# Performance work log

Hardware: AMD Instinct MI355X
Metric: run time of the kernel (lower is better)

The kernel has to match this reference:

```python
import jax, jax.numpy as jnp
import numpy as np

N = 50000      # n_samples (nodes)
F = 128        # n_features
H = 32         # hidden_dim
C = 16         # code_dim
DEG = 32       # avg degree
E = N * DEG + N  # random edges + self loops


def setup_inputs() -> dict:
    key = jax.random.key(0)
    ks = jax.random.split(key, 9)
    src = jax.random.randint(ks[0], (N * DEG,), 0, N, dtype=jnp.int32)
    dst = jax.random.randint(ks[1], (N * DEG,), 0, N, dtype=jnp.int32)
    loops = jnp.arange(N, dtype=jnp.int32)
    edge_src = jnp.concatenate([src, loops])
    edge_dst = jnp.concatenate([dst, loops])
    # symmetric normalization D^{-1/2} (A+I) D^{-1/2} on the edge list
    deg = jax.ops.segment_sum(jnp.ones((E,), jnp.float32), edge_dst, num_segments=N)
    deg = jnp.maximum(deg, 1.0)
    edge_w = jax.lax.rsqrt(deg[edge_src] * deg[edge_dst])
    rand_u = jax.random.uniform(ks[2], (N, C), jnp.float32)  # torch.rand_like
    def w(k, i, o):
        return jax.random.normal(k, (i, o), jnp.float32) * (1.0 / np.sqrt(i))
    return {
        'x': jax.random.normal(ks[3], (N, F), jnp.float32),
        'edge_src': edge_src, 'edge_dst': edge_dst, 'edge_w': edge_w,
        'rand_u': rand_u,
        'W1': w(ks[4], F, H), 'Wm': w(ks[5], H, C), 'Ws': w(ks[6], H, C),
        'Wd': w(ks[7], C, H), 'Wo': w(ks[8], H, F),
    }


def _gcn(x, W, edge_src, edge_dst, edge_w):
    # KipfAndWillingConv: spmm(A_norm, x @ W)
    support = x @ W                               # [N, out]
    msgs = edge_w[:, None] * support[edge_src]    # [E, out]
    return jax.ops.segment_sum(msgs, edge_dst, num_segments=N)


def reference(x, edge_src, edge_dst, edge_w, rand_u, W1, Wm, Ws, Wd, Wo):
    gcn = lambda h, W: _gcn(h, W, edge_src, edge_dst, edge_w)
    hidden = jax.nn.relu(gcn(x, W1))
    means = gcn(hidden, Wm)
    std = jax.nn.elu(gcn(hidden, Ws)) + 1.0
    encoded = means + std * rand_u                # uniform reparameterization
    decoded = jax.nn.relu(gcn(encoded, Wd))
    prediction = jax.nn.relu(gcn(decoded, Wo))
    return (prediction, means, std)
```

## Files before the change

### kernel.cpp

```cpp
#include <hip/hip_runtime.h>
#include <hip/hip_bf16.h>
#include <hip/hip_fp16.h>

typedef unsigned int u32;
typedef unsigned short u16;
typedef unsigned long long u64;

#define NBIN 512
#define BSH 7
#define BCAP 36
#define CHUNK 4096
#define PAD 80
#define HB 128

__global__ __launch_bounds__(64) void k_init(int* __restrict__ ovf_cnt) {
  if (threadIdx.x == 0) *ovf_cnt = 0;
}

__global__ __launch_bounds__(512) void k_bin(const int* __restrict__ src, const int* __restrict__ dst,
                                             int E2, u32* __restrict__ binned, int* __restrict__ blkcnt,
                                             u32* __restrict__ ovf, int* __restrict__ ovf_cnt, int ovfcap) {
  __shared__ int curs[NBIN];
  const int p = blockIdx.x;
  const int base = p * CHUNK;
  const int len = min(CHUNK, E2 - base);
  const int t = threadIdx.x;
  const int lane = t & 63;
  for (int i = t; i < NBIN; i += 512) curs[i] = 0;
  __syncthreads();
  const u32 blkBase = (u32)p * (NBIN * BCAP);
  for (int i = t; i < len; i += 512) {
    int d = dst[base + i];
    u32 e = ((u32)d << 16) | (u32)src[base + i];
    int b = d >> BSH;
    int pos = atomicAdd(&curs[b], 1);
    if (pos < BCAP) binned[blkBase + (u32)b * BCAP + pos] = e;
    u64 om = __ballot(pos >= BCAP);
    if (om) {
      int leader = __ffsll((long long)om) - 1;
      int ob = 0;
      if (lane == leader) ob = atomicAdd(ovf_cnt, (int)__popcll(om));
      ob = __shfl(ob, leader);
      if (pos >= BCAP) {
        int oi = ob + (int)__popcll(om & ((1ull << lane) - 1ull));
        if (oi < ovfcap) ovf[oi] = e;
      }
    }
  }
  __syncthreads();
  for (int b = t; b < NBIN; b += 512) blkcnt[p * NBIN + b] = min(curs[b], BCAP);
}

__global__ __launch_bounds__(512) void k_sort(const u32* __restrict__ binned, const int* __restrict__ blkcnt,
                                              int nblk, const u32* __restrict__ ovf,
                                              const int* __restrict__ ovf_cnt, int N,
                                              u16* __restrict__ csr, int* __restrict__ cur) {
  __shared__ __attribute__((aligned(16))) u16 scsr[HB * PAD];
  __shared__ int cnt[HB];
  const int bin = blockIdx.x;
  const int lo = bin << BSH;
  if (lo >= N) return;
  const int hi = min(lo + HB, N);
  const int H = hi - lo;
  const int t = threadIdx.x;
  const int w = t >> 6, lane = t & 63;
  for (int i = t; i < HB; i += 512) cnt[i] = 0;
  __syncthreads();
  const int per = (nblk + 7) / 8;
  const int c0 = w * per;
  const int c1 = min(nblk, c0 + per);
  const int s = lane >> 3;
  const int k = lane & 7;
  for (int p = c0; p < c1; p += 8) {
    const int myp = p + s;
    int len = 0; u32 sb = 0;
    if (myp < c1) {
      len = blkcnt[myp * NBIN + bin];
      sb = ((u32)myp * NBIN + (u32)bin) * BCAP;
    }
    for (int i = k; i < len; i += 8) {
      u32 e = binned[sb + i];
      int d = (int)(e >> 16);
      int pos = atomicAdd(&cnt[d - lo], 1);
      if (pos < PAD) scsr[(d - lo) * PAD + pos] = (u16)(e & 0xffffu);
    }
  }
  const int onum = min(*ovf_cnt, 1 << 19);
  for (int i = t; i < onum; i += 512) {
    u32 e = ovf[i];
    int d = (int)(e >> 16);
    if (d >= lo && d < hi) {
      int pos = atomicAdd(&cnt[d - lo], 1);
      if (pos < PAD) scsr[(d - lo) * PAD + pos] = (u16)(e & 0xffffu);
    }
  }
  __syncthreads();
  if (H == HB) {
    const uint4* s4 = (const uint4*)scsr;
    uint4* d4 = (uint4*)(csr + (size_t)lo * PAD);
    for (int i = t; i < HB * PAD / 8; i += 512) d4[i] = s4[i];
  } else {
    for (int i = t; i < H * (PAD / 8); i += 512) {
      int node = i / (PAD / 8), q = i % (PAD / 8);
      ((uint4*)(csr + (size_t)(lo + node) * PAD))[q] = ((const uint4*)(scsr + node * PAD))[q];
    }
  }
  for (int i = t; i < H; i += 512) cur[lo + i] = cnt[i];
}

__device__ __forceinline__ void acc8(uint4 v, float* a) {
  const __half2* h = reinterpret_cast<const __half2*>(&v);
#pragma unroll
  for (int p = 0; p < 4; ++p) {
    float2 f = __half22float2(h[p]);
    a[2 * p] += f.x;
    a[2 * p + 1] += f.y;
  }
}
__device__ __forceinline__ uint4 pack8h(const float* v) {
  uint4 r;
  __half2* h = reinterpret_cast<__half2*>(&r);
#pragma unroll
  for (int p = 0; p < 4; ++p) h[p] = __floats2half2_rn(v[2 * p], v[2 * p + 1]);
  return r;
}
__device__ __forceinline__ uint2 pack4h(const float* v) {
  uint2 r;
  __half2* h = reinterpret_cast<__half2*>(&r);
  h[0] = __floats2half2_rn(v[0], v[1]);
  h[1] = __floats2half2_rn(v[2], v[3]);
  return r;
}

template <int LPN8>
__device__ __forceinline__ void gather8h(const u16* __restrict__ csr, const int* __restrict__ cur,
                                         const float* __restrict__ dinv, const uint4* __restrict__ supv,
                                         int g, int cg, float* acc, float& dg_out) {
  int len = min(cur[g], PAD);
  const u16* c = csr + (size_t)g * PAD;
#pragma unroll
  for (int p = 0; p < 8; ++p) acc[p] = 0.f;
  acc8(supv[(size_t)g * LPN8 + cg], acc);
  int i = 0;
  for (; i + 3 < len; i += 4) {
    ushort4 ii = *(const ushort4*)(c + i);
    acc8(supv[(size_t)ii.x * LPN8 + cg], acc);
    acc8(supv[(size_t)ii.y * LPN8 + cg], acc);
    acc8(supv[(size_t)ii.z * LPN8 + cg], acc);
    acc8(supv[(size_t)ii.w * LPN8 + cg], acc);
  }
  for (; i < len; ++i) acc8(supv[(size_t)c[i] * LPN8 + cg], acc);
  float dg = dinv[g];
  dg_out = dg;
#pragma unroll
  for (int p = 0; p < 8; ++p) acc[p] *= dg;
}

__global__ __launch_bounds__(256) void k_spmm_relu(const u16* __restrict__ csr, const int* __restrict__ cur,
                                                   const float* __restrict__ dinv,
                                                   const uint4* __restrict__ sup, uint4* __restrict__ out, int N) {
  int g = blockIdx.x * 64 + (int)(threadIdx.x >> 2);
  int cg = threadIdx.x & 3;
  if (g >= N) return;
  float a[8], dg;
  gather8h<4>(csr, cur, dinv, sup, g, cg, a, dg);
#pragma unroll
  for (int p = 0; p < 8; ++p) a[p] = dg * fmaxf(a[p], 0.f);
  out[(size_t)g * 4 + cg] = pack8h(a);
}

__global__ __launch_bounds__(256) void k_spmm_ms(const u16* __restrict__ csr, const int* __restrict__ cur,
                                                  const float* __restrict__ dinv,
                                                  const uint4* __restrict__ sup,
                                                  const float* __restrict__ Wm, const float* __restrict__ Ws,
                                                  const float* __restrict__ ru,
                                                  uint2* __restrict__ enc,
                                                  float* __restrict__ o_means, float* __restrict__ o_std, int N) {
  __shared__ float w[32 * 32];
  __shared__ float aggT[64][33];
  const int t = threadIdx.x;
  for (int i = t; i < 32 * 32; i += 256) {
    int k = i >> 5, j = i & 31;
    w[i] = (j < 16) ? Wm[k * 16 + j] : Ws[k * 16 + (j - 16)];
  }
  const int n = t >> 2;
  const int q = t & 3;
  const int g = blockIdx.x * 64 + n;
  const bool act = g < N;
  float dg = 0.f, a[8];
  if (act) {
    gather8h<4>(csr, cur, dinv, sup, g, q, a, dg);
#pragma unroll
    for (int p = 0; p < 8; ++p) aggT[n][q * 8 + p] = a[p];
  }
  __syncthreads();
  if (act) {
    float4 rm = make_float4(0.f, 0.f, 0.f, 0.f);
    float4 rs = make_float4(0.f, 0.f, 0.f, 0.f);
    for (int k = 0; k < 32; ++k) {
      float rv = aggT[n][k];
      const float4* wr = (const float4*)&w[k * 32];
      float4 wm = wr[q];
      float4 wsv = wr[4 + q];
      rm.x += rv * wm.x; rm.y += rv * wm.y; rm.z += rv * wm.z; rm.w += rv * wm.w;
      rs.x += rv * wsv.x; rs.y += rv * wsv.y; rs.z += rv * wsv.z; rs.w += rv * wsv.w;
    }
    ((float4*)o_means)[(size_t)g * 4 + q] = rm;
    rs.x = ((rs.x > 0.f) ? rs.x : expm1f(rs.x)) + 1.0f;
    rs.y = ((rs.y > 0.f) ? rs.y : expm1f(rs.y)) + 1.0f;
    rs.z = ((rs.z > 0.f) ? rs.z : expm1f(rs.z)) + 1.0f;
    rs.w = ((rs.w > 0.f) ? rs.w : expm1f(rs.w)) + 1.0f;
    ((float4*)o_std)[(size_t)g * 4 + q] = rs;
    float4 uu = ((const float4*)ru)[(size_t)g * 4 + q];
    float e[4] = {dg * (rm.x + rs.x * uu.x), dg * (rm.y + rs.y * uu.y),
                  dg * (rm.z + rs.z * uu.z), dg * (rm.w + rs.w * uu.w)};
    enc[(size_t)g * 4 + q] = pack4h(e);
  }
}

__global__ __launch_bounds__(256) void k_spmm_d(const u16* __restrict__ csr, const int* __restrict__ cur,
                                                 const float* __restrict__ dinv,
                                                 const uint4* __restrict__ sup,
                                                 const float* __restrict__ Wd,
                                                 uint2* __restrict__ out, int N) {
  __shared__ float w[16 * 32];
  __shared__ float aggT[128][17];
  const int t = threadIdx.x;
  for (int i = t; i < 16 * 32; i += 256) w[i] = Wd[i];
  const int n = t >> 1;
  const int q = t & 1;
  const int g = blockIdx.x * 128 + n;
  const bool act = g < N;
  float dg = 0.f, a[8];
  if (act) {
    gather8h<2>(csr, cur, dinv, sup, g, q, a, dg);
#pragma unroll
    for (int p = 0; p < 8; ++p) aggT[n][q * 8 + p] = a[p];
  }
  __syncthreads();
  if (act) {
    float4 r4[4];
#pragma unroll
    for (int h = 0; h < 4; ++h) r4[h] = make_float4(0.f, 0.f, 0.f, 0.f);
    for (int k = 0; k < 16; ++k) {
      float rv = aggT[n][k];
      const float4* wr = (const float4*)&w[k * 32];
#pragma unroll
      for (int h = 0; h < 4; ++h) {
        float4 wv = wr[q + 2 * h];
        r4[h].x += rv * wv.x; r4[h].y += rv * wv.y;
        r4[h].z += rv * wv.z; r4[h].w += rv * wv.w;
      }
    }
#pragma unroll
    for (int h = 0; h < 4; ++h) {
      float v[4] = {dg * fmaxf(r4[h].x, 0.f), dg * fmaxf(r4[h].y, 0.f),
                    dg * fmaxf(r4[h].z, 0.f), dg * fmaxf(r4[h].w, 0.f)};
      out[(size_t)g * 8 + q + 2 * h] = pack4h(v);
    }
  }
}

__global__ __launch_bounds__(256) void k_spmm_o(const u16* __restrict__ csr, const int* __restrict__ cur,
                                                 const float* __restrict__ dinv,
                                                 const uint4* __restrict__ sup,
                                                 const float* __restrict__ Wo,
                                                 float* __restrict__ out, int N) {
  __shared__ float w[32 * 128];
  __shared__ float aggT[64][33];
  const int t = threadIdx.x;
  for (int i = t; i < 32 * 128; i += 256) w[i] = Wo[i];
  const int n = t >> 2;
  const int q = t & 3;
  const int g = blockIdx.x * 64 + n;
  const bool act = g < N;
  float dg, a[8];
  if (act) {
    gather8h<4>(csr, cur, dinv, sup, g, q, a, dg);
#pragma unroll
    for (int p = 0; p < 8; ++p) aggT[n][q * 8 + p] = a[p];
  }
  __syncthreads();
  if (act) {
    float4 r4[8];
#pragma unroll
    for (int h = 0; h < 8; ++h) r4[h] = make_float4(0.f, 0.f, 0.f, 0.f);
    for (int k = 0; k < 32; ++k) {
      float rv = aggT[n][k];
      const float4* wr = (const float4*)&w[k * 128];
#pragma unroll
      for (int h = 0; h < 8; ++h) {
        float4 wv = wr[q + 4 * h];
        r4[h].x += rv * wv.x; r4[h].y += rv * wv.y;
        r4[h].z += rv * wv.z; r4[h].w += rv * wv.w;
      }
    }
    float4* orow = (float4*)(out + (size_t)g * 128);
#pragma unroll
    for (int h = 0; h < 8; ++h)
      orow[q + 4 * h] = make_float4(fmaxf(r4[h].x, 0.f), fmaxf(r4[h].y, 0.f),
                                    fmaxf(r4[h].z, 0.f), fmaxf(r4[h].w, 0.f));
  }
}

__global__ __launch_bounds__(256) void k_mm1(const float* __restrict__ x, const float* __restrict__ W1,
                                             const int* __restrict__ cur, float* __restrict__ dinv,
                                             uint4* __restrict__ out, int N) {
  __shared__ float w[128 * 32];
  for (int i = threadIdx.x; i < 128 * 32; i += 256) w[i] = W1[i];
  __syncthreads();
  int n = blockIdx.x * 256 + threadIdx.x;
  if (n >= N) return;
  float dn = rsqrtf((float)(cur[n] + 1));
  dinv[n] = dn;
  const float4* xr = (const float4*)(x + (size_t)n * 128);
  float acc[32];
#pragma unroll
  for (int j = 0; j < 32; ++j) acc[j] = 0.f;
  for (int kb = 0; kb < 32; ++kb) {
    float4 p = xr[kb];
    float xe[4] = {p.x, p.y, p.z, p.w};
#pragma unroll
    for (int h = 0; h < 4; ++h) {
      float xv = xe[h];
      const float4* wr = (const float4*)&w[(kb * 4 + h) * 32];
#pragma unroll
      for (int q = 0; q < 8; ++q) {
        float4 a = wr[q];
        acc[q * 4 + 0] += xv * a.x; acc[q * 4 + 1] += xv * a.y;
        acc[q * 4 + 2] += xv * a.z; acc[q * 4 + 3] += xv * a.w;
      }
    }
  }
#pragma unroll
  for (int j = 0; j < 32; ++j) acc[j] *= dn;
  uint4* o = out + (size_t)n * 4;
#pragma unroll
  for (int q = 0; q < 4; ++q) o[q] = pack8h(&acc[q * 8]);
}

extern "C" void kernel_launch(void* const* d_in, const int* in_sizes, int n_in,
                              void* d_out, int out_size, void* d_ws, size_t ws_size,
                              hipStream_t stream) {
  const float* x  = (const float*)d_in[0];
  const int* esrc = (const int*)d_in[1];
  const int* edst = (const int*)d_in[2];
  const float* ru = (const float*)d_in[4];
  const float* W1 = (const float*)d_in[5];
  const float* Wm = (const float*)d_in[6];
  const float* Ws = (const float*)d_in[7];
  const float* Wd = (const float*)d_in[8];
  const float* Wo = (const float*)d_in[9];
  const int N = in_sizes[0] / 128;
  const int E = in_sizes[1];
  const int E2 = E - N;

  const int nblk = (E2 + CHUNK - 1) / CHUNK;
  const int ovfcap = 1 << 19;

  char* ws = (char*)d_ws;
  size_t off = 0;
  auto alloc = [&](size_t bytes) {
    void* p = ws + off;
    off = (off + bytes + 255) & ~(size_t)255;
    return p;
  };
  u16*   csr     = (u16*)alloc((size_t)N * PAD * 2);
  u32*   binned  = (u32*)alloc((size_t)nblk * NBIN * BCAP * 4);
  int*   blkcnt  = (int*)alloc((size_t)nblk * NBIN * 4);
  u32*   ovf     = (u32*)alloc((size_t)ovfcap * 4);
  int*   ovf_cnt = (int*)alloc(256);
  int*   cur     = (int*)alloc((size_t)N * 4);
  float* dinv    = (float*)alloc((size_t)N * 4);
  uint4* h0      = (uint4*)alloc((size_t)N * 32 * 2);
  uint4* h1      = (uint4*)alloc((size_t)N * 32 * 2);
  uint2* henc    = (uint2*)alloc((size_t)N * 16 * 2);

  float* out_pred  = (float*)d_out;
  float* out_means = out_pred + (size_t)N * 128;
  float* out_std   = out_means + (size_t)N * 16;

  const int nb = (N + 255) / 256;
  const int sortBlocks = (N + HB - 1) / HB;
  const int g64 = (N + 63) / 64;
  const int g128 = (N + 127) / 128;

  k_init<<<1, 64, 0, stream>>>(ovf_cnt);
  k_bin<<<nblk, 512, 0, stream>>>(esrc, edst, E2, binned, blkcnt, ovf, ovf_cnt, ovfcap);
  k_sort<<<sortBlocks, 512, 0, stream>>>(binned, blkcnt, nblk, ovf, ovf_cnt, N, csr, cur);

  k_mm1<<<nb, 256, 0, stream>>>(x, W1, cur, dinv, h0, N);
  k_spmm_relu<<<g64, 256, 0, stream>>>(csr, cur, dinv, h0, h1, N);
  k_spmm_ms<<<g64, 256, 0, stream>>>(csr, cur, dinv, h1, Wm, Ws, ru,
                                     henc, out_means, out_std, N);
  k_spmm_d<<<g128, 256, 0, stream>>>(csr, cur, dinv, (const uint4*)henc, Wd,
                                     (uint2*)h0, N);
  k_spmm_o<<<g64, 256, 0, stream>>>(csr, cur, dinv, h0, Wo, out_pred, N);
}
```

Measured before the change: 149.1 us.

## Split each node's neighbor gather across two thread halves with shuffle reduction

```diff
diff --git a/kernel.cpp b/kernel.cpp
--- a/kernel.cpp
+++ b/kernel.cpp
@@ -131,26 +131,34 @@
   h[1] = __floats2half2_rn(v[2], v[3]);
   return r;
 }
-
-template <int LPN8>
-__device__ __forceinline__ void gather8h(const u16* __restrict__ csr, const int* __restrict__ cur,
-                                         const float* __restrict__ dinv, const uint4* __restrict__ supv,
-                                         int g, int cg, float* acc, float& dg_out) {
+__device__ __forceinline__ u32 pack2h(float a, float b) {
+  __half2 h = __floats2half2_rn(a, b);
+  return *reinterpret_cast<u32*>(&h);
+}
+
+template <int LPN, int XD>
+__device__ __forceinline__ void gather_split(const u16* __restrict__ csr, const int* __restrict__ cur,
+                                             const float* __restrict__ dinv, const uint4* __restrict__ supv,
+                                             int g, int cg, int half, float* acc, float& dg_out) {
   int len = min(cur[g], PAD);
   const u16* c = csr + (size_t)g * PAD;
 #pragma unroll
   for (int p = 0; p < 8; ++p) acc[p] = 0.f;
-  acc8(supv[(size_t)g * LPN8 + cg], acc);
-  int i = 0;
-  for (; i + 3 < len; i += 4) {
-    ushort4 ii = *(const ushort4*)(c + i);
-    acc8(supv[(size_t)ii.x * LPN8 + cg], acc);
-    acc8(supv[(size_t)ii.y * LPN8 + cg], acc);
-    acc8(supv[(size_t)ii.z * LPN8 + cg], acc);
-    acc8(supv[(size_t)ii.w * LPN8 + cg], acc);
-  }
-  for (; i < len; ++i) acc8(supv[(size_t)c[i] * LPN8 + cg], acc);
+  if (half == 0) acc8(supv[(size_t)g * LPN + cg], acc);
+  const int full4 = len >> 2;
+  for (int j = half; j < full4; j += 2) {
+    ushort4 ii = *(const ushort4*)(c + 4 * j);
+    acc8(supv[(size_t)ii.x * LPN + cg], acc);
+    acc8(supv[(size_t)ii.y * LPN + cg], acc);
+    acc8(supv[(size_t)ii.z * LPN + cg], acc);
+    acc8(supv[(size_t)ii.w * LPN + cg], acc);
+  }
+  if ((full4 & 1) == half) {
+    for (int i = full4 << 2; i < len; ++i) acc8(supv[(size_t)c[i] * LPN + cg], acc);
+  }
   float dg = dinv[g];
+#pragma unroll
+  for (int p = 0; p < 8; ++p) acc[p] += __shfl_xor(acc[p], XD);
   dg_out = dg;
 #pragma unroll
   for (int p = 0; p < 8; ++p) acc[p] *= dg;
@@ -159,14 +167,17 @@
 __global__ __launch_bounds__(256) void k_spmm_relu(const u16* __restrict__ csr, const int* __restrict__ cur,
                                                    const float* __restrict__ dinv,
                                                    const uint4* __restrict__ sup, uint4* __restrict__ out, int N) {
-  int g = blockIdx.x * 64 + (int)(threadIdx.x >> 2);
-  int cg = threadIdx.x & 3;
+  int g = blockIdx.x * 32 + (int)(threadIdx.x >> 3);
+  int sub = threadIdx.x & 7;
+  int half = sub >> 2, cg = sub & 3;
   if (g >= N) return;
   float a[8], dg;
-  gather8h<4>(csr, cur, dinv, sup, g, cg, a, dg);
-#pragma unroll
-  for (int p = 0; p < 8; ++p) a[p] = dg * fmaxf(a[p], 0.f);
-  out[(size_t)g * 4 + cg] = pack8h(a);
+  gather_split<4, 4>(csr, cur, dinv, sup, g, cg, half, a, dg);
+  if (half == 0) {
+#pragma unroll
+    for (int p = 0; p < 8; ++p) a[p] = dg * fmaxf(a[p], 0.f);
+    out[(size_t)g * 4 + cg] = pack8h(a);
+  }
 }
 
 __global__ __launch_bounds__(256) void k_spmm_ms(const u16* __restrict__ csr, const int* __restrict__ cur,
@@ -174,47 +185,45 @@
                                                   const uint4* __restrict__ sup,
                                                   const float* __restrict__ Wm, const float* __restrict__ Ws,
                                                   const float* __restrict__ ru,
-                                                  uint2* __restrict__ enc,
+                                                  u32* __restrict__ enc,
                                                   float* __restrict__ o_means, float* __restrict__ o_std, int N) {
   __shared__ float w[32 * 32];
-  __shared__ float aggT[64][33];
+  __shared__ float aggT[32][33];
   const int t = threadIdx.x;
   for (int i = t; i < 32 * 32; i += 256) {
     int k = i >> 5, j = i & 31;
     w[i] = (j < 16) ? Wm[k * 16 + j] : Ws[k * 16 + (j - 16)];
   }
-  const int n = t >> 2;
-  const int q = t & 3;
-  const int g = blockIdx.x * 64 + n;
+  const int n = t >> 3;
+  const int sub = t & 7;
+  const int half = sub >> 2, cg = sub & 3;
+  const int g = blockIdx.x * 32 + n;
   const bool act = g < N;
   float dg = 0.f, a[8];
   if (act) {
-    gather8h<4>(csr, cur, dinv, sup, g, q, a, dg);
-#pragma unroll
-    for (int p = 0; p < 8; ++p) aggT[n][q * 8 + p] = a[p];
-  }
-  __syncthreads();
-  if (act) {
-    float4 rm = make_float4(0.f, 0.f, 0.f, 0.f);
-    float4 rs = make_float4(0.f, 0.f, 0.f, 0.f);
+    gather_split<4, 4>(csr, cur, dinv, sup, g, cg, half, a, dg);
+    if (half == 0) {
+#pragma unroll
+      for (int p = 0; p < 8; ++p) aggT[n][cg * 8 + p] = a[p];
+    }
+  }
+  __syncthreads();
+  if (act) {
+    const int q = sub;
+    float2 rm = make_float2(0.f, 0.f), rs = make_float2(0.f, 0.f);
     for (int k = 0; k < 32; ++k) {
       float rv = aggT[n][k];
-      const float4* wr = (const float4*)&w[k * 32];
-      float4 wm = wr[q];
-      float4 wsv = wr[4 + q];
-      rm.x += rv * wm.x; rm.y += rv * wm.y; rm.z += rv * wm.z; rm.w += rv * wm.w;
-      rs.x += rv * wsv.x; rs.y += rv * wsv.y; rs.z += rv * wsv.z; rs.w += rv * wsv.w;
-    }
-    ((float4*)o_means)[(size_t)g * 4 + q] = rm;
+      const float2* wr = (const float2*)&w[k * 32];
+      float2 wm = wr[q], wsv = wr[8 + q];
+      rm.x += rv * wm.x; rm.y += rv * wm.y;
+      rs.x += rv * wsv.x; rs.y += rv * wsv.y;
+    }
+    ((float2*)o_means)[(size_t)g * 8 + q] = rm;
     rs.x = ((rs.x > 0.f) ? rs.x : expm1f(rs.x)) + 1.0f;
     rs.y = ((rs.y > 0.f) ? rs.y : expm1f(rs.y)) + 1.0f;
-    rs.z = ((rs.z > 0.f) ? rs.z : expm1f(rs.z)) + 1.0f;
-    rs.w = ((rs.w > 0.f) ? rs.w : expm1f(rs.w)) + 1.0f;
-    ((float4*)o_std)[(size_t)g * 4 + q] = rs;
-    float4 uu = ((const float4*)ru)[(size_t)g * 4 + q];
-    float e[4] = {dg * (rm.x + rs.x * uu.x), dg * (rm.y + rs.y * uu.y),
-                  dg * (rm.z + rs.z * uu.z), dg * (rm.w + rs.w * uu.w)};
-    enc[(size_t)g * 4 + q] = pack4h(e);
+    ((float2*)o_std)[(size_t)g * 8 + q] = rs;
+    float2 uu = ((const float2*)ru)[(size_t)g * 8 + q];
+    enc[(size_t)g * 8 + q] = pack2h(dg * (rm.x + rs.x * uu.x), dg * (rm.y + rs.y * uu.y));
   }
 }
 
@@ -224,40 +233,40 @@
                                                  const float* __restrict__ Wd,
                                                  uint2* __restrict__ out, int N) {
   __shared__ float w[16 * 32];
-  __shared__ float aggT[128][17];
+  __shared__ float aggT[64][17];
   const int t = threadIdx.x;
   for (int i = t; i < 16 * 32; i += 256) w[i] = Wd[i];
-  const int n = t >> 1;
-  const int q = t & 1;
-  const int g = blockIdx.x * 128 + n;
+  const int n = t >> 2;
+  const int sub = t & 3;
+  const int half = sub >> 1, cg = sub & 1;
+  const int g = blockIdx.x * 64 + n;
   const bool act = g < N;
   float dg = 0.f, a[8];
   if (act) {
-    gather8h<2>(csr, cur, dinv, sup, g, q, a, dg);
-#pragma unroll
-    for (int p = 0; p < 8; ++p) aggT[n][q * 8 + p] = a[p];
-  }
-  __syncthreads();
-  if (act) {
-    float4 r4[4];
-#pragma unroll
-    for (int h = 0; h < 4; ++h) r4[h] = make_float4(0.f, 0.f, 0.f, 0.f);
+    gather_split<2, 2>(csr, cur, dinv, sup, g, cg, half, a, dg);
+    if (half == 0) {
+#pragma unroll
+      for (int p = 0; p < 8; ++p) aggT[n][cg * 8 + p] = a[p];
+    }
+  }
+  __syncthreads();
+  if (act) {
+    const int q = sub;
+    float4 r0 = make_float4(0.f, 0.f, 0.f, 0.f), r1 = r0;
     for (int k = 0; k < 16; ++k) {
       float rv = aggT[n][k];
       const float4* wr = (const float4*)&w[k * 32];
-#pragma unroll
-      for (int h = 0; h < 4; ++h) {
-        float4 wv = wr[q + 2 * h];
-        r4[h].x += rv * wv.x; r4[h].y += rv * wv.y;
-        r4[h].z += rv * wv.z; r4[h].w += rv * wv.w;
-      }
-    }
-#pragma unroll
-    for (int h = 0; h < 4; ++h) {
-      float v[4] = {dg * fmaxf(r4[h].x, 0.f), dg * fmaxf(r4[h].y, 0.f),
-                    dg * fmaxf(r4[h].z, 0.f), dg * fmaxf(r4[h].w, 0.f)};
-      out[(size_t)g * 8 + q + 2 * h] = pack4h(v);
-    }
+      float4 w0 = wr[q], w1 = wr[q + 4];
+      r0.x += rv * w0.x; r0.y += rv * w0.y; r0.z += rv * w0.z; r0.w += rv * w0.w;
+      r1.x += rv * w1.x; r1.y += rv * w1.y; r1.z += rv * w1.z; r1.w += rv * w1.w;
+    }
+    float v[4];
+    v[0] = dg * fmaxf(r0.x, 0.f); v[1] = dg * fmaxf(r0.y, 0.f);
+    v[2] = dg * fmaxf(r0.z, 0.f); v[3] = dg * fmaxf(r0.w, 0.f);
+    out[(size_t)g * 8 + q] = pack4h(v);
+    v[0] = dg * fmaxf(r1.x, 0.f); v[1] = dg * fmaxf(r1.y, 0.f);
+    v[2] = dg * fmaxf(r1.z, 0.f); v[3] = dg * fmaxf(r1.w, 0.f);
+    out[(size_t)g * 8 + q + 4] = pack4h(v);
   }
 }
 
@@ -267,38 +276,42 @@
                                                  const float* __restrict__ Wo,
                                                  float* __restrict__ out, int N) {
   __shared__ float w[32 * 128];
-  __shared__ float aggT[64][33];
+  __shared__ float aggT[32][33];
   const int t = threadIdx.x;
   for (int i = t; i < 32 * 128; i += 256) w[i] = Wo[i];
-  const int n = t >> 2;
-  const int q = t & 3;
-  const int g = blockIdx.x * 64 + n;
+  const int n = t >> 3;
+  const int sub = t & 7;
+  const int half = sub >> 2, cg = sub & 3;
+  const int g = blockIdx.x * 32 + n;
   const bool act = g < N;
   float dg, a[8];
   if (act) {
-    gather8h<4>(csr, cur, dinv, sup, g, q, a, dg);
-#pragma unroll
-    for (int p = 0; p < 8; ++p) aggT[n][q * 8 + p] = a[p];
-  }
-  __syncthreads();
-  if (act) {
-    float4 r4[8];
-#pragma unroll
-    for (int h = 0; h < 8; ++h) r4[h] = make_float4(0.f, 0.f, 0.f, 0.f);
+    gather_split<4, 4>(csr, cur, dinv, sup, g, cg, half, a, dg);
+    if (half == 0) {
+#pragma unroll
+      for (int p = 0; p < 8; ++p) aggT[n][cg * 8 + p] = a[p];
+    }
+  }
+  __syncthreads();
+  if (act) {
+    const int q = sub;
+    float4 r4[4];
+#pragma unroll
+    for (int h = 0; h < 4; ++h) r4[h] = make_float4(0.f, 0.f, 0.f, 0.f);
     for (int k = 0; k < 32; ++k) {
       float rv = aggT[n][k];
       const float4* wr = (const float4*)&w[k * 128];
 #pragma unroll
-      for (int h = 0; h < 8; ++h) {
-        float4 wv = wr[q + 4 * h];
+      for (int h = 0; h < 4; ++h) {
+        float4 wv = wr[q + 8 * h];
         r4[h].x += rv * wv.x; r4[h].y += rv * wv.y;
         r4[h].z += rv * wv.z; r4[h].w += rv * wv.w;
       }
     }
     float4* orow = (float4*)(out + (size_t)g * 128);
 #pragma unroll
-    for (int h = 0; h < 8; ++h)
-      orow[q + 4 * h] = make_float4(fmaxf(r4[h].x, 0.f), fmaxf(r4[h].y, 0.f),
+    for (int h = 0; h < 4; ++h)
+      orow[q + 8 * h] = make_float4(fmaxf(r4[h].x, 0.f), fmaxf(r4[h].y, 0.f),
                                     fmaxf(r4[h].z, 0.f), fmaxf(r4[h].w, 0.f));
   }
 }
@@ -374,7 +387,7 @@
   float* dinv    = (float*)alloc((size_t)N * 4);
   uint4* h0      = (uint4*)alloc((size_t)N * 32 * 2);
   uint4* h1      = (uint4*)alloc((size_t)N * 32 * 2);
-  uint2* henc    = (uint2*)alloc((size_t)N * 16 * 2);
+  u32*   henc    = (u32*)alloc((size_t)N * 16 * 2);
 
   float* out_pred  = (float*)d_out;
   float* out_means = out_pred + (size_t)N * 128;
@@ -382,18 +395,18 @@
 
   const int nb = (N + 255) / 256;
   const int sortBlocks = (N + HB - 1) / HB;
+  const int g32 = (N + 31) / 32;
   const int g64 = (N + 63) / 64;
-  const int g128 = (N + 127) / 128;
 
   k_init<<<1, 64, 0, stream>>>(ovf_cnt);
   k_bin<<<nblk, 512, 0, stream>>>(esrc, edst, E2, binned, blkcnt, ovf, ovf_cnt, ovfcap);
   k_sort<<<sortBlocks, 512, 0, stream>>>(binned, blkcnt, nblk, ovf, ovf_cnt, N, csr, cur);
 
   k_mm1<<<nb, 256, 0, stream>>>(x, W1, cur, dinv, h0, N);
-  k_spmm_relu<<<g64, 256, 0, stream>>>(csr, cur, dinv, h0, h1, N);
-  k_spmm_ms<<<g64, 256, 0, stream>>>(csr, cur, dinv, h1, Wm, Ws, ru,
+  k_spmm_relu<<<g32, 256, 0, stream>>>(csr, cur, dinv, h0, h1, N);
+  k_spmm_ms<<<g32, 256, 0, stream>>>(csr, cur, dinv, h1, Wm, Ws, ru,
                                      henc, out_means, out_std, N);
-  k_spmm_d<<<g128, 256, 0, stream>>>(csr, cur, dinv, (const uint4*)henc, Wd,
-                                     (uint2*)h0, N);
-  k_spmm_o<<<g64, 256, 0, stream>>>(csr, cur, dinv, h0, Wo, out_pred, N);
-}
+  k_spmm_d<<<g64, 256, 0, stream>>>(csr, cur, dinv, (const uint4*)henc, Wd,
+                                    (uint2*)h0, N);
+  k_spmm_o<<<g32, 256, 0, stream>>>(csr, cur, dinv, h0, Wo, out_pred, N);
+}
```

Result: faster. 140.6 us (-5.7%).
